# Performance work log

Measured on AMD Instinct MI355X. Metric: run time of the kernel, lower is better.

The kernel has to match this reference:

```python
import jax, jax.numpy as jnp
import numpy as np

B, N, M, DIN, H = 8, 2048, 2048, 512, 256
SCALE = float(np.sqrt(H))


def _lin_params(key, din, dout):
    kw, kb = jax.random.split(key)
    lim = 1.0 / np.sqrt(din)
    W = jax.random.uniform(kw, (din, dout), jnp.float32, -lim, lim)
    b = jax.random.uniform(kb, (dout,), jnp.float32, -lim, lim)
    return W, b


def setup_inputs() -> dict:
    key = jax.random.key(0)
    ks = jax.random.split(key, 16)
    inp = {
        "q_fp": jax.random.normal(ks[0], (B, N, DIN), jnp.float32),
        "v_ret": jax.random.normal(ks[1], (B, M, DIN), jnp.float32),
        "pi_star": jax.random.uniform(ks[2], (B, N, M), jnp.float32),
    }
    names = ["qs", "ks", "vs", "qe", "ke", "ve"]
    for i, nm in enumerate(names):
        W, b = _lin_params(ks[3 + i], DIN, H)
        inp[f"W{nm}"], inp[f"b{nm}"] = W, b
    inp["W1"], inp["b1"] = _lin_params(ks[10], 4 * H, H)
    inp["W2"], inp["b2"] = _lin_params(ks[11], H, H)
    inp["gamma"] = jnp.ones((1,), jnp.float32)
    inp["ew"] = jnp.array(1.0, jnp.float32)
    return inp


def _forward(q_fp, v_ret, pi_star, Wqs, bqs, Wks, bks, Wvs, bvs,
             Wqe, bqe, Wke, bke, Wve, bve, W1, b1, W2, b2, gamma, ew):
    q_struct = q_fp @ Wqs + bqs          # [B,N,H]
    k_struct = v_ret @ Wks + bks         # [B,M,H]
    v_struct = v_ret @ Wvs + bvs
    q_elec = q_fp @ Wqe + bqe
    k_elec = v_ret @ Wke + bke
    v_elec = v_ret @ Wve + bve

    structural_logits = jnp.einsum("bnh,bmh->bnm", q_struct, k_struct) / SCALE

    # cdist(p=2) via the quadratic expansion, clamped for numeric safety
    q2 = jnp.sum(q_elec * q_elec, -1, keepdims=True)          # [B,N,1]
    k2 = jnp.sum(k_elec * k_elec, -1, keepdims=True)          # [B,M,1]
    d2 = q2 + jnp.swapaxes(k2, -2, -1) - 2.0 * jnp.einsum("bnh,bmh->bnm", q_elec, k_elec)
    electronic_distance = jnp.sqrt(jnp.maximum(d2, 1e-12))    # [B,N,M]
    electronic_scale = jnp.maximum(
        electronic_distance.mean(axis=(-2, -1), keepdims=True), 1e-4)
    electronic_logits = -(electronic_distance / electronic_scale)

    pi_mask = gamma * jnp.log(jnp.maximum(pi_star, 1e-9))
    final_logits = structural_logits + ew * electronic_logits + pi_mask
    attn = jax.nn.softmax(final_logits, axis=-1)              # [B,N,M]

    ctx_s = jnp.einsum("bnm,bmh->bnh", attn, v_struct)
    ctx_e = jnp.einsum("bnm,bmh->bnh", attn, v_elec)
    fused = jnp.concatenate([ctx_s, ctx_e, ctx_s - ctx_e, ctx_s * ctx_e], axis=-1)
    h = jax.nn.silu(fused @ W1 + b1)
    return h @ W2 + b2


def reference(q_fp, v_ret, pi_star, Wqs, bqs, Wks, bks, Wvs, bvs,
              Wqe, bqe, Wke, bke, Wve, bve, W1, b1, W2, b2, gamma, ew):
    return _forward(q_fp, v_ret, pi_star, Wqs, bqs, Wks, bks, Wvs, bvs,
                    Wqe, bqe, Wke, bke, Wve, bve, W1, b1, W2, b2, gamma, ew)
```

## Files before the change

kernel.cpp:

```cpp
#include <hip/hip_runtime.h>

#define Bsz 8
#define Nq  2048
#define Mk  2048
#define BKt 32

typedef __attribute__((ext_vector_type(8))) short   short8;
typedef __attribute__((ext_vector_type(4))) float   floatx4;

__device__ __forceinline__ unsigned short f2bf(float f) {
  union { float f; unsigned u; } x; x.f = f;
  unsigned r = x.u + 0x7fffu + ((x.u >> 16) & 1u);
  return (unsigned short)(r >> 16);
}
__device__ __forceinline__ float bf2f(unsigned short s) {
  union { unsigned u; float f; } x; x.u = ((unsigned)s) << 16;
  return x.f;
}

__device__ __forceinline__ void async16(const unsigned short* g, unsigned short* l) {
  __builtin_amdgcn_global_load_lds(
      (const __attribute__((address_space(1))) unsigned int*)g,
      (__attribute__((address_space(3))) unsigned int*)l, 16, 0, 0);
}

__device__ __forceinline__ void gemm_core_nt(
    const unsigned short* __restrict__ A, int lda,
    const unsigned short* __restrict__ B, int ldb,
    int K, unsigned short* ldsA, unsigned short* ldsB,
    floatx4 (&acc)[4][4])
{
  const int tid  = threadIdx.x;
  const int lane = tid & 63;
  const int sr   = tid >> 2;
  const int sc   = (tid & 3) << 3;
  const int wid  = tid >> 6;
  const int wm   = wid & 1;
  const int wn   = wid >> 1;
  const int fr   = lane & 15;
  const int fk   = (lane >> 4) << 3;

  const unsigned short* a0p = A + (size_t)sr * lda + sc;
  const unsigned short* a1p = A + (size_t)(sr + 64) * lda + sc;
  const unsigned short* b0p = B + (size_t)sr * ldb + sc;
  const unsigned short* b1p = B + (size_t)(sr + 64) * ldb + sc;
  unsigned short* la0 = ldsA + tid * 8;
  unsigned short* la1 = ldsA + 2048 + tid * 8;
  unsigned short* lb0 = ldsB + tid * 8;
  unsigned short* lb1 = ldsB + 2048 + tid * 8;
  const unsigned short* fa = ldsA + (wm * 64 + fr) * BKt + fk;
  const unsigned short* fb = ldsB + (wn * 64 + fr) * BKt + fk;

  for (int k0 = 0; k0 < K; k0 += BKt) {
    __syncthreads();
    async16(a0p, la0); a0p += BKt;
    async16(a1p, la1); a1p += BKt;
    async16(b0p, lb0); b0p += BKt;
    async16(b1p, lb1); b1p += BKt;
    __syncthreads();
    short8 af[4], bfr[4];
#pragma unroll
    for (int i = 0; i < 4; i++) af[i]  = *(const short8*)(fa + i * 16 * BKt);
#pragma unroll
    for (int i = 0; i < 4; i++) bfr[i] = *(const short8*)(fb + i * 16 * BKt);
#pragma unroll
    for (int i = 0; i < 4; i++)
#pragma unroll
      for (int j = 0; j < 4; j++)
        acc[i][j] = __builtin_amdgcn_mfma_f32_16x16x32_bf16(af[i], bfr[j], acc[i][j], 0, 0, 0);
  }
}

#define EPILOGUE_VARS \
  const int lane = threadIdx.x & 63; \
  const int wid  = threadIdx.x >> 6; \
  const int wm   = wid & 1; \
  const int wn   = wid >> 1; \
  const int r4   = (lane >> 4) * 4;  \
  const int cn   = lane & 15; \
  (void)wid;

template<int MODE>
__global__ __launch_bounds__(256) void k_gemm_bias(
    const unsigned short* __restrict__ A, const unsigned short* __restrict__ Bw,
    const float* __restrict__ bias, void* __restrict__ Cout, int Ncols, int K)
{
  __shared__ alignas(16) unsigned short ldsA[128 * BKt];
  __shared__ alignas(16) unsigned short ldsB[128 * BKt];
  floatx4 acc[4][4];
#pragma unroll
  for (int i = 0; i < 4; i++)
#pragma unroll
    for (int j = 0; j < 4; j++)
#pragma unroll
      for (int t = 0; t < 4; t++) acc[i][j][t] = 0.f;

  const unsigned short* Ab = A + (size_t)blockIdx.x * 128 * K;
  const unsigned short* Bb = Bw + (size_t)blockIdx.y * 128 * K;
  gemm_core_nt(Ab, K, Bb, K, K, ldsA, ldsB, acc);

  EPILOGUE_VARS
#pragma unroll
  for (int i = 0; i < 4; i++) {
#pragma unroll
    for (int j = 0; j < 4; j++) {
      int gc = blockIdx.y * 128 + wn * 64 + j * 16 + cn;
      float bv = bias[gc];
#pragma unroll
      for (int r = 0; r < 4; r++) {
        int gr = blockIdx.x * 128 + wm * 64 + i * 16 + r4 + r;
        float v = acc[i][j][r] + bv;
        if constexpr (MODE == 1) v = v / (1.f + __expf(-v));
        if constexpr (MODE == 2)
          ((float*)Cout)[(size_t)gr * Ncols + gc] = v;
        else
          ((unsigned short*)Cout)[(size_t)gr * Ncols + gc] = f2bf(v);
      }
    }
  }
}

__global__ __launch_bounds__(256) void k_pass1(
    const unsigned short* __restrict__ Xq, const unsigned short* __restrict__ Xk,
    const float* __restrict__ q2, const float* __restrict__ k2,
    float* __restrict__ dsum, float* __restrict__ rowsum)
{
  {
    int blin = (blockIdx.z * 16 + blockIdx.y) * 16 + blockIdx.x;
    if (threadIdx.x < 8) rowsum[blin * 8 + threadIdx.x] = 0.f;
  }
  __shared__ alignas(16) unsigned short ldsA[128 * BKt];
  __shared__ alignas(16) unsigned short ldsB[128 * BKt];
  floatx4 acc[4][4];
#pragma unroll
  for (int i = 0; i < 4; i++)
#pragma unroll
    for (int j = 0; j < 4; j++)
#pragma unroll
      for (int t = 0; t < 4; t++) acc[i][j][t] = 0.f;

  const int b = blockIdx.z;
  const unsigned short* Ab = Xq + ((size_t)(b * Nq) + blockIdx.x * 128) * 512 + 256;
  const unsigned short* Bb = Xk + ((size_t)(b * Mk) + blockIdx.y * 128) * 1024 + 512;
  gemm_core_nt(Ab, 512, Bb, 1024, 256, ldsA, ldsB, acc);

  EPILOGUE_VARS
  const int rowBase = b * Nq + blockIdx.x * 128;
  const int colBase = b * Mk + blockIdx.y * 128;
  float lsum = 0.f;
#pragma unroll
  for (int i = 0; i < 4; i++) {
#pragma unroll
    for (int j = 0; j < 4; j++) {
      float kk = k2[colBase + wn * 64 + j * 16 + cn];
#pragma unroll
      for (int r = 0; r < 4; r++) {
        float qq = q2[rowBase + wm * 64 + i * 16 + r4 + r];
        float d2 = qq + kk - 2.f * acc[i][j][r];
        lsum += sqrtf(fmaxf(d2, 1e-12f));
      }
    }
  }
#pragma unroll
  for (int o = 32; o; o >>= 1) lsum += __shfl_down(lsum, o);
  __syncthreads();
  float* red = (float*)ldsA;
  if (lane == 0) red[wid] = lsum;
  __syncthreads();
  if (threadIdx.x == 0) atomicAdd(dsum + b, red[0] + red[1] + red[2] + red[3]);
}

__global__ __launch_bounds__(256) void k_logits(
    const unsigned short* __restrict__ Xq, const unsigned short* __restrict__ Xk,
    const float* __restrict__ q2, const float* __restrict__ k2,
    const float* __restrict__ dsum, const float* __restrict__ pi,
    const float* __restrict__ gamma_p, const float* __restrict__ ew_p,
    unsigned short* __restrict__ attn, float* __restrict__ rowsum)
{
  __shared__ alignas(16) unsigned short ldsA[128 * BKt];
  __shared__ alignas(16) unsigned short ldsB[128 * BKt];
  floatx4 accS[4][4], accE[4][4];
#pragma unroll
  for (int i = 0; i < 4; i++)
#pragma unroll
    for (int j = 0; j < 4; j++)
#pragma unroll
      for (int t = 0; t < 4; t++) { accS[i][j][t] = 0.f; accE[i][j][t] = 0.f; }

  const int b = blockIdx.z;
  const unsigned short* Aq_s = Xq + ((size_t)(b * Nq) + blockIdx.x * 128) * 512;
  const unsigned short* Bk_s = Xk + ((size_t)(b * Mk) + blockIdx.y * 128) * 1024;
  gemm_core_nt(Aq_s,       512, Bk_s,       1024, 256, ldsA, ldsB, accS);
  gemm_core_nt(Aq_s + 256, 512, Bk_s + 512, 1024, 256, ldsA, ldsB, accE);

  const float scale = fmaxf(dsum[b] * (1.f / (2048.f * 2048.f)), 1e-4f);
  const float einv  = ew_p[0] / scale;
  const float gv    = gamma_p[0];

  EPILOGUE_VARS
  float rs[4][4];
#pragma unroll
  for (int i = 0; i < 4; i++)
#pragma unroll
    for (int r = 0; r < 4; r++) rs[i][r] = 0.f;

#pragma unroll
  for (int i = 0; i < 4; i++) {
#pragma unroll
    for (int j = 0; j < 4; j++) {
      int m = blockIdx.y * 128 + wn * 64 + j * 16 + cn;
      float kk = k2[b * Mk + m];
#pragma unroll
      for (int r = 0; r < 4; r++) {
        int n = blockIdx.x * 128 + wm * 64 + i * 16 + r4 + r;
        float qq = q2[b * Nq + n];
        float d  = sqrtf(fmaxf(qq + kk - 2.f * accE[i][j][r], 1e-12f));
        float p  = pi[((size_t)b * Nq + n) * Mk + m];
        float l  = accS[i][j][r] * 0.0625f - einv * d + gv * __logf(fmaxf(p, 1e-9f));
        float e  = __expf(l);
        rs[i][r] += e;
        attn[((size_t)b * Nq + n) * Mk + m] = f2bf(e);
      }
    }
  }
#pragma unroll
  for (int i = 0; i < 4; i++)
#pragma unroll
    for (int r = 0; r < 4; r++) {
      float v = rs[i][r];
      v += __shfl_xor(v, 1); v += __shfl_xor(v, 2);
      v += __shfl_xor(v, 4); v += __shfl_xor(v, 8);
      if (cn == 0)
        atomicAdd(rowsum + b * Nq + blockIdx.x * 128 + wm * 64 + i * 16 + r4 + r, v);
    }
}

__global__ __launch_bounds__(256) void k_pv(
    const unsigned short* __restrict__ At, const unsigned short* __restrict__ VT,
    const float* __restrict__ rowsum, unsigned short* __restrict__ ctx)
{
  __shared__ alignas(16) unsigned short ldsA[128 * BKt];
  __shared__ alignas(16) unsigned short ldsB[128 * BKt];
  floatx4 acc[4][4];
#pragma unroll
  for (int i = 0; i < 4; i++)
#pragma unroll
    for (int j = 0; j < 4; j++)
#pragma unroll
      for (int t = 0; t < 4; t++) acc[i][j][t] = 0.f;

  const int b = blockIdx.z;
  const unsigned short* Ab = At + ((size_t)b * Nq + blockIdx.x * 128) * (size_t)Mk;
  const unsigned short* Bb = VT + ((size_t)b * 512 + blockIdx.y * 128) * (size_t)Mk;
  gemm_core_nt(Ab, Mk, Bb, Mk, Mk, ldsA, ldsB, acc);

  EPILOGUE_VARS
  const int rowbase = b * Nq + blockIdx.x * 128 + wm * 64;
  float rinv[4][4];
#pragma unroll
  for (int i = 0; i < 4; i++)
#pragma unroll
    for (int r = 0; r < 4; r++)
      rinv[i][r] = 1.f / rowsum[rowbase + i * 16 + r4 + r];
#pragma unroll
  for (int i = 0; i < 4; i++)
#pragma unroll
    for (int j = 0; j < 4; j++) {
      int gc = blockIdx.y * 128 + wn * 64 + j * 16 + cn;
#pragma unroll
      for (int r = 0; r < 4; r++) {
        int gr = blockIdx.x * 128 + wm * 64 + i * 16 + r4 + r;
        ctx[((size_t)b * Nq + gr) * 512 + gc] = f2bf(acc[i][j][r] * rinv[i][r]);
      }
    }
}

__global__ void k_f32_bf16(const float* __restrict__ src, unsigned short* __restrict__ dst) {
  size_t i = ((size_t)blockIdx.x * 256 + threadIdx.x) * 4;
  float4 v = *(const float4*)(src + i);
  uint2 o;
  o.x = f2bf(v.x) | ((unsigned)f2bf(v.y) << 16);
  o.y = f2bf(v.z) | ((unsigned)f2bf(v.w) << 16);
  *(uint2*)(dst + i) = o;
}

__global__ void k_prep_w(
    const float* __restrict__ Wqs, const float* __restrict__ Wqe,
    const float* __restrict__ Wks, const float* __restrict__ Wvs,
    const float* __restrict__ Wke, const float* __restrict__ Wve,
    const float* __restrict__ W1,  const float* __restrict__ W2,
    const float* __restrict__ bqs, const float* __restrict__ bqe,
    const float* __restrict__ bks, const float* __restrict__ bvs,
    const float* __restrict__ bke, const float* __restrict__ bve,
    unsigned short* __restrict__ WqT, unsigned short* __restrict__ WkT,
    unsigned short* __restrict__ W1T, unsigned short* __restrict__ W2T,
    float* __restrict__ bq, float* __restrict__ bk, float* __restrict__ dsum)
{
  int gid = blockIdx.x * 256 + threadIdx.x;
  int idx = gid;
  if (idx < 512 * 512) {
    int j = idx >> 9, k = idx & 511;
    float v = (j < 256) ? Wqs[k * 256 + j] : Wqe[k * 256 + (j - 256)];
    WqT[idx] = f2bf(v);
  } else if ((idx -= 512 * 512) < 1024 * 512) {
    int j = idx >> 9, k = idx & 511;
    int s = j >> 8, jj = j & 255;
    const float* Wp = (s == 0) ? Wks : (s == 1) ? Wvs : (s == 2) ? Wke : Wve;
    WkT[idx] = f2bf(Wp[k * 256 + jj]);
  } else if ((idx -= 1024 * 512) < 256 * 1024) {
    int j = idx >> 10, k = idx & 1023;
    W1T[idx] = f2bf(W1[k * 256 + j]);
  } else if ((idx -= 256 * 1024) < 256 * 256) {
    int j = idx >> 8, k = idx & 255;
    W2T[idx] = f2bf(W2[k * 256 + j]);
  }
  if (gid < 512)  bq[gid] = (gid < 256) ? bqs[gid] : bqe[gid - 256];
  if (gid < 1024) bk[gid] = (gid < 256) ? bks[gid]
                    : (gid < 512) ? bvs[gid - 256]
                    : (gid < 768) ? bke[gid - 512] : bve[gid - 768];
  if (gid < 8) dsum[gid] = 0.f;
}

__global__ __launch_bounds__(256) void k_rowsq(
    const unsigned short* __restrict__ X, int stride, int colOff, float* __restrict__ out)
{
  int row = blockIdx.x * 4 + (threadIdx.x >> 6);
  int lane = threadIdx.x & 63;
  const unsigned short* p = X + (size_t)row * stride + colOff + lane * 4;
  uint2 u = *(const uint2*)p;
  float a0 = bf2f((unsigned short)(u.x & 0xffff));
  float a1 = bf2f((unsigned short)(u.x >> 16));
  float a2 = bf2f((unsigned short)(u.y & 0xffff));
  float a3 = bf2f((unsigned short)(u.y >> 16));
  float s = a0 * a0 + a1 * a1 + a2 * a2 + a3 * a3;
#pragma unroll
  for (int o = 32; o; o >>= 1) s += __shfl_down(s, o);
  if (lane == 0) out[row] = s;
}

__global__ void k_trans_vt(const unsigned short* __restrict__ Xk, unsigned short* __restrict__ VT) {
  __shared__ unsigned short t[32][33];
  const int b = blockIdx.z;
  const int m0 = blockIdx.x * 32, j0 = blockIdx.y * 32;
  const int tx = threadIdx.x, ty = threadIdx.y;
#pragma unroll
  for (int i = 0; i < 4; i++) {
    int m = m0 + ty + i * 8;
    int j = j0 + tx;
    int c = (j < 256) ? (256 + j) : (512 + j);
    t[ty + i * 8][tx] = Xk[((size_t)b * Mk + m) * 1024 + c];
  }
  __syncthreads();
#pragma unroll
  for (int i = 0; i < 4; i++) {
    int j = j0 + ty + i * 8;
    int m = m0 + tx;
    VT[((size_t)b * 512 + j) * Mk + m] = t[tx][ty + i * 8];
  }
}

__global__ void k_fused(const unsigned short* __restrict__ ctx, unsigned short* __restrict__ fused) {
  int idx = blockIdx.x * 256 + threadIdx.x;
  int bn = idx >> 8;
  int j = idx & 255;
  float cs = bf2f(ctx[(size_t)bn * 512 + j]);
  float ce = bf2f(ctx[(size_t)bn * 512 + 256 + j]);
  size_t o = (size_t)bn * 1024 + j;
  fused[o]       = f2bf(cs);
  fused[o + 256] = f2bf(ce);
  fused[o + 512] = f2bf(cs - ce);
  fused[o + 768] = f2bf(cs * ce);
}

extern "C" void kernel_launch(void* const* d_in, const int* in_sizes, int n_in,
                              void* d_out, int out_size, void* d_ws, size_t ws_size,
                              hipStream_t stream) {
  (void)in_sizes; (void)n_in; (void)out_size; (void)ws_size;
  const float* q_fp  = (const float*)d_in[0];
  const float* v_ret = (const float*)d_in[1];
  const float* pi    = (const float*)d_in[2];
  const float* Wqs = (const float*)d_in[3];  const float* bqs = (const float*)d_in[4];
  const float* Wks = (const float*)d_in[5];  const float* bks = (const float*)d_in[6];
  const float* Wvs = (const float*)d_in[7];  const float* bvs = (const float*)d_in[8];
  const float* Wqe = (const float*)d_in[9];  const float* bqe = (const float*)d_in[10];
  const float* Wke = (const float*)d_in[11]; const float* bke = (const float*)d_in[12];
  const float* Wve = (const float*)d_in[13]; const float* bve = (const float*)d_in[14];
  const float* W1  = (const float*)d_in[15]; const float* b1  = (const float*)d_in[16];
  const float* W2  = (const float*)d_in[17]; const float* b2  = (const float*)d_in[18];
  const float* gamma = (const float*)d_in[19];
  const float* ew    = (const float*)d_in[20];

  char* w = (char*)d_ws;
  unsigned short* WqT = (unsigned short*)(w + 0);
  unsigned short* WkT = (unsigned short*)(w + 524288);
  unsigned short* W1T = (unsigned short*)(w + 1572864);
  unsigned short* W2T = (unsigned short*)(w + 2097152);
  float* bq   = (float*)(w + 2228224);
  float* bk   = (float*)(w + 2230272);
  float* q2   = (float*)(w + 2234368);
  float* k2   = (float*)(w + 2299904);
  float* dsum = (float*)(w + 2365440);
  unsigned short* Aq = (unsigned short*)(w + 2365696);
  unsigned short* Ak = (unsigned short*)(w + 19142912);
  unsigned short* Xq = (unsigned short*)(w + 35920128);
  unsigned short* Xk = (unsigned short*)(w + 52697344);
  unsigned short* VT = (unsigned short*)(w + 86251776);
  unsigned short* attn = (unsigned short*)(w + 103028992);
  unsigned short* ctx  = Aq;
  unsigned short* fused = (unsigned short*)(w + 103028992);
  unsigned short* hbuf  = Ak;
  float* rowsum = (float*)d_out;

  k_f32_bf16<<<8192, 256, 0, stream>>>(q_fp, Aq);
  k_f32_bf16<<<8192, 256, 0, stream>>>(v_ret, Ak);
  k_prep_w<<<4352, 256, 0, stream>>>(Wqs, Wqe, Wks, Wvs, Wke, Wve, W1, W2,
                                     bqs, bqe, bks, bvs, bke, bve,
                                     WqT, WkT, W1T, W2T, bq, bk, dsum);
  k_gemm_bias<0><<<dim3(128, 4), 256, 0, stream>>>(Aq, WqT, bq, Xq, 512, 512);
  k_gemm_bias<0><<<dim3(128, 8), 256, 0, stream>>>(Ak, WkT, bk, Xk, 1024, 512);
  k_rowsq<<<4096, 256, 0, stream>>>(Xq, 512, 256, q2);
  k_rowsq<<<4096, 256, 0, stream>>>(Xk, 1024, 512, k2);
  k_pass1<<<dim3(16, 16, 8), 256, 0, stream>>>(Xq, Xk, q2, k2, dsum, rowsum);
  k_logits<<<dim3(16, 16, 8), 256, 0, stream>>>(Xq, Xk, q2, k2, dsum, pi, gamma, ew,
                                                attn, rowsum);
  k_trans_vt<<<dim3(64, 16, 8), dim3(32, 8), 0, stream>>>(Xk, VT);
  k_pv<<<dim3(16, 4, 8), 256, 0, stream>>>(attn, VT, rowsum, ctx);
  k_fused<<<16384, 256, 0, stream>>>(ctx, fused);
  k_gemm_bias<1><<<dim3(128, 2), 256, 0, stream>>>(fused, W1T, b1, hbuf, 256, 1024);
  k_gemm_bias<2><<<dim3(128, 2), 256, 0, stream>>>(hbuf, W2T, b2, d_out, 256, 256);
}
```

Baseline: 671.0 us.

## Fuse input casts into projection GEMMs, retile PV, simplify logits exp

Measured after the change: 685.3 us. +2.1%, slower.

```diff
diff --git a/kernel.cpp b/kernel.cpp
--- a/kernel.cpp
+++ b/kernel.cpp
@@ -16,12 +16,6 @@
 __device__ __forceinline__ float bf2f(unsigned short s) {
   union { unsigned u; float f; } x; x.u = ((unsigned)s) << 16;
   return x.f;
-}
-
-__device__ __forceinline__ void async16(const unsigned short* g, unsigned short* l) {
-  __builtin_amdgcn_global_load_lds(
-      (const __attribute__((address_space(1))) unsigned int*)g,
-      (__attribute__((address_space(3))) unsigned int*)l, 16, 0, 0);
 }
 
 __device__ __forceinline__ void gemm_core_nt(
@@ -44,19 +38,20 @@
   const unsigned short* a1p = A + (size_t)(sr + 64) * lda + sc;
   const unsigned short* b0p = B + (size_t)sr * ldb + sc;
   const unsigned short* b1p = B + (size_t)(sr + 64) * ldb + sc;
-  unsigned short* la0 = ldsA + tid * 8;
-  unsigned short* la1 = ldsA + 2048 + tid * 8;
-  unsigned short* lb0 = ldsB + tid * 8;
-  unsigned short* lb1 = ldsB + 2048 + tid * 8;
+  uint4* sa0 = (uint4*)(ldsA + sr * BKt + sc);
+  uint4* sa1 = (uint4*)(ldsA + (sr + 64) * BKt + sc);
+  uint4* sb0 = (uint4*)(ldsB + sr * BKt + sc);
+  uint4* sb1 = (uint4*)(ldsB + (sr + 64) * BKt + sc);
   const unsigned short* fa = ldsA + (wm * 64 + fr) * BKt + fk;
   const unsigned short* fb = ldsB + (wn * 64 + fr) * BKt + fk;
 
   for (int k0 = 0; k0 < K; k0 += BKt) {
+    uint4 a0 = *(const uint4*)a0p; a0p += BKt;
+    uint4 a1 = *(const uint4*)a1p; a1p += BKt;
+    uint4 b0 = *(const uint4*)b0p; b0p += BKt;
+    uint4 b1 = *(const uint4*)b1p; b1p += BKt;
     __syncthreads();
-    async16(a0p, la0); a0p += BKt;
-    async16(a1p, la1); a1p += BKt;
-    async16(b0p, lb0); b0p += BKt;
-    async16(b1p, lb1); b1p += BKt;
+    *sa0 = a0; *sa1 = a1; *sb0 = b0; *sb1 = b1;
     __syncthreads();
     short8 af[4], bfr[4];
 #pragma unroll
@@ -79,6 +74,93 @@
   const int r4   = (lane >> 4) * 4;  \
   const int cn   = lane & 15; \
   (void)wid;
+
+__global__ __launch_bounds__(256) void k_proj(
+    const float* __restrict__ A, const unsigned short* __restrict__ Bw,
+    const float* __restrict__ bias, unsigned short* __restrict__ Cout,
+    int Ncols, int K)
+{
+  __shared__ alignas(16) unsigned short ldsA[128 * BKt];
+  __shared__ alignas(16) unsigned short ldsB[128 * BKt];
+  floatx4 acc[4][4];
+#pragma unroll
+  for (int i = 0; i < 4; i++)
+#pragma unroll
+    for (int j = 0; j < 4; j++)
+#pragma unroll
+      for (int t = 0; t < 4; t++) acc[i][j][t] = 0.f;
+
+  const int tid = threadIdx.x;
+  const int ar  = tid >> 1;
+  const int ac  = (tid & 1) << 4;
+  const int sr  = tid >> 2;
+  const int sc  = (tid & 3) << 3;
+
+  const float* ap = A + ((size_t)blockIdx.x * 128 + ar) * K + ac;
+  const unsigned short* b0p = Bw + ((size_t)blockIdx.y * 128 + sr) * K + sc;
+  const unsigned short* b1p = b0p + (size_t)64 * K;
+  uint4* sa  = (uint4*)(ldsA + ar * BKt + ac);
+  uint4* sb0 = (uint4*)(ldsB + sr * BKt + sc);
+  uint4* sb1 = (uint4*)(ldsB + (sr + 64) * BKt + sc);
+
+  {
+    const int lane = tid & 63;
+    const int wm   = (tid >> 6) & 1;
+    const int wn   = tid >> 7;
+    const int fr   = lane & 15;
+    const int fk   = (lane >> 4) << 3;
+    const unsigned short* fa = ldsA + (wm * 64 + fr) * BKt + fk;
+    const unsigned short* fb = ldsB + (wn * 64 + fr) * BKt + fk;
+
+    for (int k0 = 0; k0 < K; k0 += BKt) {
+      float4 f0 = *(const float4*)(ap + 0);
+      float4 f1 = *(const float4*)(ap + 4);
+      float4 f2 = *(const float4*)(ap + 8);
+      float4 f3 = *(const float4*)(ap + 12);
+      ap += BKt;
+      uint4 b0 = *(const uint4*)b0p; b0p += BKt;
+      uint4 b1 = *(const uint4*)b1p; b1p += BKt;
+      uint4 pa, pb;
+      pa.x = f2bf(f0.x) | ((unsigned)f2bf(f0.y) << 16);
+      pa.y = f2bf(f0.z) | ((unsigned)f2bf(f0.w) << 16);
+      pa.z = f2bf(f1.x) | ((unsigned)f2bf(f1.y) << 16);
+      pa.w = f2bf(f1.z) | ((unsigned)f2bf(f1.w) << 16);
+      pb.x = f2bf(f2.x) | ((unsigned)f2bf(f2.y) << 16);
+      pb.y = f2bf(f2.z) | ((unsigned)f2bf(f2.w) << 16);
+      pb.z = f2bf(f3.x) | ((unsigned)f2bf(f3.y) << 16);
+      pb.w = f2bf(f3.z) | ((unsigned)f2bf(f3.w) << 16);
+      __syncthreads();
+      sa[0] = pa; sa[1] = pb;
+      *sb0 = b0; *sb1 = b1;
+      __syncthreads();
+      short8 af[4], bfr[4];
+#pragma unroll
+      for (int i = 0; i < 4; i++) af[i]  = *(const short8*)(fa + i * 16 * BKt);
+#pragma unroll
+      for (int i = 0; i < 4; i++) bfr[i] = *(const short8*)(fb + i * 16 * BKt);
+#pragma unroll
+      for (int i = 0; i < 4; i++)
+#pragma unroll
+        for (int j = 0; j < 4; j++)
+          acc[i][j] = __builtin_amdgcn_mfma_f32_16x16x32_bf16(af[i], bfr[j], acc[i][j], 0, 0, 0);
+    }
+  }
+
+  EPILOGUE_VARS
+#pragma unroll
+  for (int i = 0; i < 4; i++) {
+#pragma unroll
+    for (int j = 0; j < 4; j++) {
+      int gc = blockIdx.y * 128 + wn * 64 + j * 16 + cn;
+      float bv = bias[gc];
+#pragma unroll
+      for (int r = 0; r < 4; r++) {
+        int gr = blockIdx.x * 128 + wm * 64 + i * 16 + r4 + r;
+        Cout[(size_t)gr * Ncols + gc] = f2bf(acc[i][j][r] + bv);
+      }
+    }
+  }
+}
 
 template<int MODE>
 __global__ __launch_bounds__(256) void k_gemm_bias(
@@ -156,8 +238,7 @@
 #pragma unroll
       for (int r = 0; r < 4; r++) {
         float qq = q2[rowBase + wm * 64 + i * 16 + r4 + r];
-        float d2 = qq + kk - 2.f * acc[i][j][r];
-        lsum += sqrtf(fmaxf(d2, 1e-12f));
+        lsum += sqrtf(fmaxf(qq + kk - 2.f * acc[i][j][r], 1e-12f));
       }
     }
   }
@@ -196,6 +277,7 @@
   const float scale = fmaxf(dsum[b] * (1.f / (2048.f * 2048.f)), 1e-4f);
   const float einv  = ew_p[0] / scale;
   const float gv    = gamma_p[0];
+  const bool  g1    = (gv == 1.0f);
 
   EPILOGUE_VARS
   float rs[4][4];
@@ -214,12 +296,13 @@
       for (int r = 0; r < 4; r++) {
         int n = blockIdx.x * 128 + wm * 64 + i * 16 + r4 + r;
         float qq = q2[b * Nq + n];
+        size_t idx = ((size_t)b * Nq + n) * Mk + m;
         float d  = sqrtf(fmaxf(qq + kk - 2.f * accE[i][j][r], 1e-12f));
-        float p  = pi[((size_t)b * Nq + n) * Mk + m];
-        float l  = accS[i][j][r] * 0.0625f - einv * d + gv * __logf(fmaxf(p, 1e-9f));
-        float e  = __expf(l);
+        float p  = fmaxf(pi[idx], 1e-9f);
+        float pf = g1 ? p : __expf(gv * __logf(p));
+        float e  = __expf(accS[i][j][r] * 0.0625f - einv * d) * pf;
         rs[i][r] += e;
-        attn[((size_t)b * Nq + n) * Mk + m] = f2bf(e);
+        attn[idx] = f2bf(e);
       }
     }
   }
@@ -240,21 +323,56 @@
     const float* __restrict__ rowsum, unsigned short* __restrict__ ctx)
 {
   __shared__ alignas(16) unsigned short ldsA[128 * BKt];
-  __shared__ alignas(16) unsigned short ldsB[128 * BKt];
-  floatx4 acc[4][4];
-#pragma unroll
-  for (int i = 0; i < 4; i++)
-#pragma unroll
-    for (int j = 0; j < 4; j++)
+  __shared__ alignas(16) unsigned short ldsB[64 * BKt];
+  floatx4 acc[4][2];
+#pragma unroll
+  for (int i = 0; i < 4; i++)
+#pragma unroll
+    for (int j = 0; j < 2; j++)
 #pragma unroll
       for (int t = 0; t < 4; t++) acc[i][j][t] = 0.f;
 
   const int b = blockIdx.z;
-  const unsigned short* Ab = At + ((size_t)b * Nq + blockIdx.x * 128) * (size_t)Mk;
-  const unsigned short* Bb = VT + ((size_t)b * 512 + blockIdx.y * 128) * (size_t)Mk;
-  gemm_core_nt(Ab, Mk, Bb, Mk, Mk, ldsA, ldsB, acc);
-
-  EPILOGUE_VARS
+  const int tid  = threadIdx.x;
+  const int lane = tid & 63;
+  const int sr   = tid >> 2;
+  const int sc   = (tid & 3) << 3;
+  const int wid  = tid >> 6;
+  const int wm   = wid & 1;
+  const int wn   = wid >> 1;
+  const int fr   = lane & 15;
+  const int fk   = (lane >> 4) << 3;
+
+  const unsigned short* a0p = At + ((size_t)b * Nq + blockIdx.x * 128 + sr) * Mk + sc;
+  const unsigned short* a1p = a0p + (size_t)64 * Mk;
+  const unsigned short* bp  = VT + ((size_t)b * 512 + blockIdx.y * 64 + sr) * Mk + sc;
+  uint4* sa0 = (uint4*)(ldsA + sr * BKt + sc);
+  uint4* sa1 = (uint4*)(ldsA + (sr + 64) * BKt + sc);
+  uint4* sb  = (uint4*)(ldsB + sr * BKt + sc);
+  const unsigned short* fa = ldsA + (wm * 64 + fr) * BKt + fk;
+  const unsigned short* fb = ldsB + (wn * 32 + fr) * BKt + fk;
+
+  for (int k0 = 0; k0 < Mk; k0 += BKt) {
+    uint4 a0 = *(const uint4*)a0p; a0p += BKt;
+    uint4 a1 = *(const uint4*)a1p; a1p += BKt;
+    uint4 b0 = *(const uint4*)bp;  bp  += BKt;
+    __syncthreads();
+    *sa0 = a0; *sa1 = a1; *sb = b0;
+    __syncthreads();
+    short8 af[4], bfr[2];
+#pragma unroll
+    for (int i = 0; i < 4; i++) af[i]  = *(const short8*)(fa + i * 16 * BKt);
+#pragma unroll
+    for (int j = 0; j < 2; j++) bfr[j] = *(const short8*)(fb + j * 16 * BKt);
+#pragma unroll
+    for (int i = 0; i < 4; i++)
+#pragma unroll
+      for (int j = 0; j < 2; j++)
+        acc[i][j] = __builtin_amdgcn_mfma_f32_16x16x32_bf16(af[i], bfr[j], acc[i][j], 0, 0, 0);
+  }
+
+  const int r4 = (lane >> 4) * 4;
+  const int cn = lane & 15;
   const int rowbase = b * Nq + blockIdx.x * 128 + wm * 64;
   float rinv[4][4];
 #pragma unroll
@@ -265,23 +383,14 @@
 #pragma unroll
   for (int i = 0; i < 4; i++)
 #pragma unroll
-    for (int j = 0; j < 4; j++) {
-      int gc = blockIdx.y * 128 + wn * 64 + j * 16 + cn;
+    for (int j = 0; j < 2; j++) {
+      int gc = blockIdx.y * 64 + wn * 32 + j * 16 + cn;
 #pragma unroll
       for (int r = 0; r < 4; r++) {
         int gr = blockIdx.x * 128 + wm * 64 + i * 16 + r4 + r;
         ctx[((size_t)b * Nq + gr) * 512 + gc] = f2bf(acc[i][j][r] * rinv[i][r]);
       }
     }
-}
-
-__global__ void k_f32_bf16(const float* __restrict__ src, unsigned short* __restrict__ dst) {
-  size_t i = ((size_t)blockIdx.x * 256 + threadIdx.x) * 4;
-  float4 v = *(const float4*)(src + i);
-  uint2 o;
-  o.x = f2bf(v.x) | ((unsigned)f2bf(v.y) << 16);
-  o.y = f2bf(v.z) | ((unsigned)f2bf(v.w) << 16);
-  *(uint2*)(dst + i) = o;
 }
 
 __global__ void k_prep_w(
@@ -400,31 +509,27 @@
   float* q2   = (float*)(w + 2234368);
   float* k2   = (float*)(w + 2299904);
   float* dsum = (float*)(w + 2365440);
-  unsigned short* Aq = (unsigned short*)(w + 2365696);
-  unsigned short* Ak = (unsigned short*)(w + 19142912);
+  unsigned short* ctx  = (unsigned short*)(w + 2365696);
+  unsigned short* hbuf = (unsigned short*)(w + 19142912);
   unsigned short* Xq = (unsigned short*)(w + 35920128);
   unsigned short* Xk = (unsigned short*)(w + 52697344);
   unsigned short* VT = (unsigned short*)(w + 86251776);
   unsigned short* attn = (unsigned short*)(w + 103028992);
-  unsigned short* ctx  = Aq;
-  unsigned short* fused = (unsigned short*)(w + 103028992);
-  unsigned short* hbuf  = Ak;
+  unsigned short* fused = attn;
   float* rowsum = (float*)d_out;
 
-  k_f32_bf16<<<8192, 256, 0, stream>>>(q_fp, Aq);
-  k_f32_bf16<<<8192, 256, 0, stream>>>(v_ret, Ak);
   k_prep_w<<<4352, 256, 0, stream>>>(Wqs, Wqe, Wks, Wvs, Wke, Wve, W1, W2,
                                      bqs, bqe, bks, bvs, bke, bve,
                                      WqT, WkT, W1T, W2T, bq, bk, dsum);
-  k_gemm_bias<0><<<dim3(128, 4), 256, 0, stream>>>(Aq, WqT, bq, Xq, 512, 512);
-  k_gemm_bias<0><<<dim3(128, 8), 256, 0, stream>>>(Ak, WkT, bk, Xk, 1024, 512);
+  k_proj<<<dim3(128, 4), 256, 0, stream>>>(q_fp,  WqT, bq, Xq, 512, 512);
+  k_proj<<<dim3(128, 8), 256, 0, stream>>>(v_ret, WkT, bk, Xk, 1024, 512);
   k_rowsq<<<4096, 256, 0, stream>>>(Xq, 512, 256, q2);
   k_rowsq<<<4096, 256, 0, stream>>>(Xk, 1024, 512, k2);
   k_pass1<<<dim3(16, 16, 8), 256, 0, stream>>>(Xq, Xk, q2, k2, dsum, rowsum);
   k_logits<<<dim3(16, 16, 8), 256, 0, stream>>>(Xq, Xk, q2, k2, dsum, pi, gamma, ew,
                                                 attn, rowsum);
   k_trans_vt<<<dim3(64, 16, 8), dim3(32, 8), 0, stream>>>(Xk, VT);
-  k_pv<<<dim3(16, 4, 8), 256, 0, stream>>>(attn, VT, rowsum, ctx);
+  k_pv<<<dim3(16, 8, 8), 256, 0, stream>>>(attn, VT, rowsum, ctx);
   k_fused<<<16384, 256, 0, stream>>>(ctx, fused);
   k_gemm_bias<1><<<dim3(128, 2), 256, 0, stream>>>(fused, W1T, b1, hbuf, 256, 1024);
   k_gemm_bias<2><<<dim3(128, 2), 256, 0, stream>>>(hbuf, W2T, b2, d_out, 256, 256);
```
